# Optimization experiments

Hardware: AMD Instinct MI355X
Metric: run time of the kernel (lower is better)

Reference implementation:

```python
import jax, jax.numpy as jnp
import numpy as np

THRESHOLD = 0.3
STRENGTH = 0.1
MIN_S = 0.0
MAX_S = 0.5
EPS_COS = 1e-8
EPS_LN = 1e-5

B, T, D = 1024, 64, 256
P = 2048
H = 512


def _layernorm(x, g, b):
    mu = x.mean(-1, keepdims=True)
    var = ((x - mu) ** 2).mean(-1, keepdims=True)
    return (x - mu) * jax.lax.rsqrt(var + EPS_LN) * g + b


def setup_inputs() -> dict:
    key = jax.random.key(0)
    ks = jax.random.split(key, 10)
    s = lambda fan_in: 1.0 / np.sqrt(fan_in)
    return {
        "current_feat": jax.random.normal(ks[0], (B, T, D), jnp.float32),
        "prototype": jax.random.normal(ks[1], (P, T, D), jnp.float32),
        "dd_w1": jax.random.normal(ks[2], (2 * D, H), jnp.float32) * s(2 * D),
        "dd_b1": jnp.zeros((H,), jnp.float32),
        "dd_g1": jnp.ones((H,), jnp.float32),
        "dd_be1": jnp.zeros((H,), jnp.float32),
        "dd_w2": jax.random.normal(ks[3], (H, H // 2), jnp.float32) * s(H),
        "dd_b2": jnp.zeros((H // 2,), jnp.float32),
        "dd_w3": jax.random.normal(ks[4], (H // 2, 1), jnp.float32) * s(H // 2),
        "dd_b3": jnp.zeros((1,), jnp.float32),
        "cal_w1": jax.random.normal(ks[5], (D, H), jnp.float32) * s(D),
        "cal_b1": jnp.zeros((H,), jnp.float32),
        "cal_g1": jnp.ones((H,), jnp.float32),
        "cal_be1": jnp.zeros((H,), jnp.float32),
        "cal_w2": jax.random.normal(ks[6], (H, H), jnp.float32) * s(H),
        "cal_b2": jnp.zeros((H,), jnp.float32),
        "cal_w3": jax.random.normal(ks[7], (H, D), jnp.float32) * s(H),
        "cal_b3": jnp.zeros((D,), jnp.float32),
    }


def reference(current_feat, prototype,
              dd_w1, dd_b1, dd_g1, dd_be1, dd_w2, dd_b2, dd_w3, dd_b3,
              cal_w1, cal_b1, cal_g1, cal_be1, cal_w2, cal_b2, cal_w3, cal_b3):
    # --- drift detection ---
    feat_flat = current_feat.mean(axis=1)          # [B, D]
    proto_centers = prototype.mean(axis=1)         # [P, D]
    fn = jnp.maximum(jnp.linalg.norm(feat_flat, axis=-1), EPS_COS)   # [B]
    pn = jnp.maximum(jnp.linalg.norm(proto_centers, axis=-1), EPS_COS)  # [P]
    sim = jnp.einsum('bd,pd->bp', feat_flat, proto_centers) / (fn[:, None] * pn[None, :])
    drift_score = 1.0 - sim                        # [B, P]
    is_drifted = drift_score.mean(axis=0) > THRESHOLD  # [P] bool

    # --- calibration (batched over all P, then masked scatter) ---
    global_mean = feat_flat.mean(axis=0)           # [D]
    concat = jnp.concatenate(
        [proto_centers, jnp.broadcast_to(global_mean, (proto_centers.shape[0], global_mean.shape[0]))], axis=-1)  # [P, 2D]
    h = jax.nn.relu(_layernorm(concat @ dd_w1 + dd_b1, dd_g1, dd_be1))
    h = jax.nn.relu(h @ dd_w2 + dd_b2)
    drift_conf = jax.nn.sigmoid(h @ dd_w3 + dd_b3)[:, 0]  # [P]

    c = jax.nn.relu(_layernorm(proto_centers @ cal_w1 + cal_b1, cal_g1, cal_be1))
    c = jax.nn.relu(c @ cal_w2 + cal_b2)
    delta = c @ cal_w3 + cal_b3                    # [P, D]

    strength = jnp.clip(STRENGTH * drift_conf, MIN_S, MAX_S)  # [P]
    new_center = proto_centers + strength[:, None] * delta    # [P, D]

    calibrated = jnp.where(is_drifted[:, None, None], new_center[:, None, :], prototype)  # [P, T, D]
    return calibrated, drift_score, is_drifted
```

## Files before the change

### kernel.cpp

```cpp
#include <hip/hip_runtime.h>
#include <hip/hip_bf16.h>
#include <math.h>

#define BB 1024
#define TT 64
#define DD 256
#define PP 2048
#define HH 512

typedef __attribute__((ext_vector_type(8))) short short8;
typedef __attribute__((ext_vector_type(4))) short short4v;
typedef __attribute__((ext_vector_type(4))) float f32x4;

__device__ __forceinline__ float4 f4add(float4 a, float4 b) {
    return make_float4(a.x + b.x, a.y + b.y, a.z + b.z, a.w + b.w);
}

__device__ __forceinline__ void nt_store4(float* p, float4 v) {
    f32x4 t = {v.x, v.y, v.z, v.w};
    __builtin_nontemporal_store(t, (f32x4*)p);
}

__device__ __forceinline__ void nt_store1(float* p, float v) {
    __builtin_nontemporal_store(v, p);
}

__device__ __forceinline__ float4 nt_load4(const float* p) {
    f32x4 t = __builtin_nontemporal_load((const f32x4*)p);
    return make_float4(t.x, t.y, t.z, t.w);
}

__device__ __forceinline__ void store_bf16x4(__hip_bfloat16* dst, float4 m) {
    union { __hip_bfloat16 h[4]; short4v s; } u;
    u.h[0] = __float2bfloat16(m.x); u.h[1] = __float2bfloat16(m.y);
    u.h[2] = __float2bfloat16(m.z); u.h[3] = __float2bfloat16(m.w);
    *(short4v*)dst = u.s;
}

__global__ void prep_k(const float* __restrict__ cf, const float* __restrict__ proto,
                       const float* __restrict__ dd_w1, const float* __restrict__ dd_w2,
                       const float* __restrict__ cal_w1, const float* __restrict__ cal_w2,
                       const float* __restrict__ cal_w3,
                       float* __restrict__ ffm, float* __restrict__ fn,
                       float* __restrict__ pn, float* __restrict__ pc,
                       float* __restrict__ colsum,
                       __hip_bfloat16* __restrict__ ffb, __hip_bfloat16* __restrict__ pcb,
                       __hip_bfloat16* __restrict__ w1cat, __hip_bfloat16* __restrict__ w2dd,
                       __hip_bfloat16* __restrict__ w2cal, __hip_bfloat16* __restrict__ w3cal) {
    int b = blockIdx.x, tid = threadIdx.x;
    if (b < 768) {
        int wv = tid >> 6, lane = tid & 63;
        int row = (b << 2) + wv;
        const float* base = (row < 1024) ? cf + (size_t)row * TT * DD
                                         : proto + (size_t)(row - 1024) * TT * DD;
        const float* p = base + (lane << 2);
        float4 acc = make_float4(0.f, 0.f, 0.f, 0.f);
        float4 v[16];
        #pragma unroll
        for (int tb = 0; tb < TT; tb += 16) {
            #pragma unroll
            for (int i = 0; i < 16; ++i)
                v[i] = nt_load4(p + (size_t)(tb + i) * DD);
            #pragma unroll
            for (int i = 0; i < 8; ++i) v[i] = f4add(v[i], v[i + 8]);
            #pragma unroll
            for (int i = 0; i < 4; ++i) v[i] = f4add(v[i], v[i + 4]);
            acc = f4add(acc, f4add(f4add(v[0], v[1]), f4add(v[2], v[3])));
        }
        float4 m = make_float4(acc.x * (1.f / TT), acc.y * (1.f / TT),
                               acc.z * (1.f / TT), acc.w * (1.f / TT));
        if (row < 1024) {
            *(float4*)(ffm + (size_t)row * DD + (lane << 2)) = m;
            store_bf16x4(ffb + (size_t)row * DD + (lane << 2), m);
        } else {
            int r = row - 1024;
            *(float4*)(pc + (size_t)r * DD + (lane << 2)) = m;
            store_bf16x4(pcb + (size_t)r * DD + (lane << 2), m);
        }
        float q = m.x * m.x + m.y * m.y + m.z * m.z + m.w * m.w;
        #pragma unroll
        for (int o = 32; o > 0; o >>= 1) q += __shfl_xor(q, o, 64);
        if (lane == 0) {
            float nv = fmaxf(sqrtf(q), 1e-8f);
            if (row < 1024) fn[row] = nv; else pn[row - 1024] = nv;
        }
    } else {
        int bb = b - 768;
        if (bb < 8) colsum[bb * 256 + tid] = 0.f;
        #pragma unroll
        for (int i2 = 0; i2 < 4; ++i2) {
            int idx = bb * 1024 + i2 * 256 + tid;
            if (idx < 262144) {
                int half = idx >> 17;
                int i = idx & 131071;
                int n = i & 511, k = i >> 9;
                const float* src = half ? cal_w1 : dd_w1;
                float x = __builtin_nontemporal_load(src + (size_t)k * 512 + n);
                w1cat[(size_t)(half * 512 + n) * 256 + k] = __float2bfloat16(x);
            } else if (idx < 393216) {
                int i = idx - 262144;
                int n = i & 255, k = i >> 8;
                float x = __builtin_nontemporal_load(dd_w2 + (size_t)k * 256 + n);
                w2dd[(size_t)n * 512 + k] = __float2bfloat16(x);
            } else if (idx < 655360) {
                int i = idx - 393216;
                int n = i & 511, k = i >> 9;
                float x = __builtin_nontemporal_load(cal_w2 + (size_t)k * 512 + n);
                w2cal[(size_t)n * 512 + k] = __float2bfloat16(x);
            } else {
                int i = idx - 655360;
                int n = i & 255, k = i >> 8;
                float x = __builtin_nontemporal_load(cal_w3 + (size_t)k * 256 + n);
                w3cal[(size_t)n * 512 + k] = __float2bfloat16(x);
            }
        }
    }
}

__global__ void sim_addvec_k(const __hip_bfloat16* __restrict__ A,
                             const __hip_bfloat16* __restrict__ Bt,
                             const float* __restrict__ fn, const float* __restrict__ pn,
                             const float* __restrict__ ffm,
                             const float* __restrict__ dd_w1, const float* __restrict__ dd_b1,
                             float* __restrict__ drift, float* __restrict__ colsum,
                             float* __restrict__ addvec) {
    if (blockIdx.x >= 512) {
        __shared__ float gmk[256];
        int tid = threadIdx.x;
        const float* f = ffm + tid;
        float a0 = 0.f, a1 = 0.f, a2 = 0.f, a3 = 0.f, a4 = 0.f, a5 = 0.f, a6 = 0.f, a7 = 0.f;
        #pragma unroll 4
        for (int b = 0; b < 1024; b += 8) {
            a0 += f[(b + 0) << 8]; a1 += f[(b + 1) << 8];
            a2 += f[(b + 2) << 8]; a3 += f[(b + 3) << 8];
            a4 += f[(b + 4) << 8]; a5 += f[(b + 5) << 8];
            a6 += f[(b + 6) << 8]; a7 += f[(b + 7) << 8];
        }
        gmk[tid] = (((a0 + a1) + (a2 + a3)) + ((a4 + a5) + (a6 + a7))) * (1.f / BB);
        __syncthreads();
        int j = (blockIdx.x - 512) * 256 + tid;
        float s = dd_b1[j];
        #pragma unroll 8
        for (int k = 0; k < 256; ++k) s = fmaf(gmk[k], dd_w1[(size_t)(256 + k) * 512 + j], s);
        addvec[j] = s;
        return;
    }
    int wid = (blockIdx.x << 2) + (threadIdx.x >> 6);
    int lane = threadIdx.x & 63;
    int mw = wid >> 6, nw = wid & 63;
    int m0 = mw << 5, n0 = nw << 5;
    int lr = lane & 15, quad = lane >> 4;
    const __hip_bfloat16* pa0 = A + (size_t)(m0 + lr) * DD + quad * 8;
    const __hip_bfloat16* pa1 = pa0 + 16 * DD;
    const __hip_bfloat16* pb0 = Bt + (size_t)(n0 + lr) * DD + quad * 8;
    const __hip_bfloat16* pb1 = pb0 + 16 * DD;
    f32x4 acc00 = {0,0,0,0}, acc01 = {0,0,0,0}, acc10 = {0,0,0,0}, acc11 = {0,0,0,0};
    #pragma unroll
    for (int k = 0; k < DD; k += 32) {
        short8 a0 = *(const short8*)(pa0 + k);
        short8 a1 = *(const short8*)(pa1 + k);
        short8 b0 = *(const short8*)(pb0 + k);
        short8 b1 = *(const short8*)(pb1 + k);
        acc00 = __builtin_amdgcn_mfma_f32_16x16x32_bf16(a0, b0, acc00, 0, 0, 0);
        acc01 = __builtin_amdgcn_mfma_f32_16x16x32_bf16(a0, b1, acc01, 0, 0, 0);
        acc10 = __builtin_amdgcn_mfma_f32_16x16x32_bf16(a1, b0, acc10, 0, 0, 0);
        acc11 = __builtin_amdgcn_mfma_f32_16x16x32_bf16(a1, b1, acc11, 0, 0, 0);
    }
    int col0 = n0 + lr, col1 = col0 + 16;
    float ip0 = 1.f / pn[col0], ip1 = 1.f / pn[col1];
    float cs0 = 0.f, cs1 = 0.f;
    #pragma unroll
    for (int r = 0; r < 4; ++r) {
        int row0 = m0 + quad * 4 + r;
        int row1 = row0 + 16;
        float if0 = 1.f / fn[row0];
        float if1 = 1.f / fn[row1];
        float d00 = 1.f - acc00[r] * if0 * ip0;
        float d01 = 1.f - acc01[r] * if0 * ip1;
        float d10 = 1.f - acc10[r] * if1 * ip0;
        float d11 = 1.f - acc11[r] * if1 * ip1;
        nt_store1(&drift[(size_t)row0 * PP + col0], d00);
        nt_store1(&drift[(size_t)row0 * PP + col1], d01);
        nt_store1(&drift[(size_t)row1 * PP + col0], d10);
        nt_store1(&drift[(size_t)row1 * PP + col1], d11);
        cs0 += d00 + d10;
        cs1 += d01 + d11;
    }
    cs0 += __shfl_xor(cs0, 16, 64); cs0 += __shfl_xor(cs0, 32, 64);
    cs1 += __shfl_xor(cs1, 16, 64); cs1 += __shfl_xor(cs1, 32, 64);
    if (quad == 0) {
        atomicAdd(&colsum[col0], cs0);
        atomicAdd(&colsum[col1], cs1);
    }
}

#define LS 520
__global__ void __launch_bounds__(256)
mlp_k(const __hip_bfloat16* __restrict__ pcb,
      const __hip_bfloat16* __restrict__ w1cat,
      const float* __restrict__ addvec, const float* __restrict__ cal_b1,
      const float* __restrict__ gdd, const float* __restrict__ bedd,
      const float* __restrict__ gcal, const float* __restrict__ becal,
      const __hip_bfloat16* __restrict__ w2dd, const __hip_bfloat16* __restrict__ w2cal,
      const float* __restrict__ dd_b2, const float* __restrict__ cal_b2,
      const __hip_bfloat16* __restrict__ w3cal, const float* __restrict__ cal_b3,
      const float* __restrict__ dd_w3, const float* __restrict__ dd_b3,
      float* __restrict__ delta, float* __restrict__ strength) {
    __shared__ __hip_bfloat16 act1[32 * LS];
    __shared__ __hip_bfloat16 act2[32 * LS];
    __shared__ float lds_s[4][32];
    __shared__ float lds_q[4][32];

    int h  = blockIdx.x & 1;
    int r0 = (blockIdx.x >> 1) << 5;
    int wv = threadIdx.x >> 6;
    int lane = threadIdx.x & 63;
    int lr = lane & 15, quad = lane >> 4;

    const float* bias1 = h ? cal_b1 : addvec;
    const float* g  = h ? gcal : gdd;
    const float* be = h ? becal : bedd;

    const __hip_bfloat16* pa0 = pcb + (size_t)(r0 + lr) * DD + quad * 8;
    const __hip_bfloat16* pa1 = pa0 + 16 * DD;
    f32x4 a00[4], a01[4], a10[4], a11[4];
    float bi0[4], bi1[4];
    #pragma unroll
    for (int t = 0; t < 4; ++t) {
        int n0g = h * 512 + wv * 128 + t * 32;
        const __hip_bfloat16* pb0 = w1cat + (size_t)(n0g + lr) * DD + quad * 8;
        const __hip_bfloat16* pb1 = pb0 + 16 * DD;
        f32x4 c00 = {0,0,0,0}, c01 = {0,0,0,0}, c10 = {0,0,0,0}, c11 = {0,0,0,0};
        #pragma unroll
        for (int k = 0; k < DD; k += 32) {
            short8 av0 = *(const short8*)(pa0 + k);
            short8 av1 = *(const short8*)(pa1 + k);
            short8 bv0 = *(const short8*)(pb0 + k);
            short8 bv1 = *(const short8*)(pb1 + k);
            c00 = __builtin_amdgcn_mfma_f32_16x16x32_bf16(av0, bv0, c00, 0, 0, 0);
            c01 = __builtin_amdgcn_mfma_f32_16x16x32_bf16(av0, bv1, c01, 0, 0, 0);
            c10 = __builtin_amdgcn_mfma_f32_16x16x32_bf16(av1, bv0, c10, 0, 0, 0);
            c11 = __builtin_amdgcn_mfma_f32_16x16x32_bf16(av1, bv1, c11, 0, 0, 0);
        }
        a00[t] = c00; a01[t] = c01; a10[t] = c10; a11[t] = c11;
        int cl0 = wv * 128 + t * 32 + lr;
        bi0[t] = bias1[cl0];
        bi1[t] = bias1[cl0 + 16];
    }
    float ps_lo[4] = {0,0,0,0}, pq_lo[4] = {0,0,0,0};
    float ps_hi[4] = {0,0,0,0}, pq_hi[4] = {0,0,0,0};
    #pragma unroll
    for (int t = 0; t < 4; ++t) {
        #pragma unroll
        for (int r = 0; r < 4; ++r) {
            float v00 = a00[t][r] + bi0[t];
            float v01 = a01[t][r] + bi1[t];
            float v10 = a10[t][r] + bi0[t];
            float v11 = a11[t][r] + bi1[t];
            a00[t][r] = v00; a01[t][r] = v01; a10[t][r] = v10; a11[t][r] = v11;
            ps_lo[r] += v00 + v01;  pq_lo[r] += v00 * v00 + v01 * v01;
            ps_hi[r] += v10 + v11;  pq_hi[r] += v10 * v10 + v11 * v11;
        }
    }
    #pragma unroll
    for (int mset = 1; mset < 16; mset <<= 1) {
        #pragma unroll
        for (int r = 0; r < 4; ++r) {
            ps_lo[r] += __shfl_xor(ps_lo[r], mset, 64);
            pq_lo[r] += __shfl_xor(pq_lo[r], mset, 64);
            ps_hi[r] += __shfl_xor(ps_hi[r], mset, 64);
            pq_hi[r] += __shfl_xor(pq_hi[r], mset, 64);
        }
    }
    if (lr < 8) {
        int rr = quad * 4 + (lr & 3) + ((lr >> 2) << 4);
        lds_s[wv][rr] = (lr >= 4) ? ps_hi[lr & 3] : ps_lo[lr & 3];
        lds_q[wv][rr] = (lr >= 4) ? pq_hi[lr & 3] : pq_lo[lr & 3];
    }
    __syncthreads();

    float mu_lo[4], rs_lo[4], mu_hi[4], rs_hi[4];
    #pragma unroll
    for (int r = 0; r < 4; ++r) {
        int rl = quad * 4 + r;
        float s = lds_s[0][rl] + lds_s[1][rl] + lds_s[2][rl] + lds_s[3][rl];
        float q = lds_q[0][rl] + lds_q[1][rl] + lds_q[2][rl] + lds_q[3][rl];
        float mu = s * (1.f / HH);
        float var = fmaxf(q * (1.f / HH) - mu * mu, 0.f);
        mu_lo[r] = mu; rs_lo[r] = rsqrtf(var + 1e-5f);
        int rh = rl + 16;
        s = lds_s[0][rh] + lds_s[1][rh] + lds_s[2][rh] + lds_s[3][rh];
        q = lds_q[0][rh] + lds_q[1][rh] + lds_q[2][rh] + lds_q[3][rh];
        mu = s * (1.f / HH);
        var = fmaxf(q * (1.f / HH) - mu * mu, 0.f);
        mu_hi[r] = mu; rs_hi[r] = rsqrtf(var + 1e-5f);
    }
    #pragma unroll
    for (int t = 0; t < 4; ++t) {
        int c0 = wv * 128 + t * 32 + lr, c1 = c0 + 16;
        float g0 = g[c0], g1 = g[c1], b0 = be[c0], b1 = be[c1];
        #pragma unroll
        for (int r = 0; r < 4; ++r) {
            int rl = quad * 4 + r, rh = rl + 16;
            act1[rl * LS + c0] = __float2bfloat16(fmaxf((a00[t][r] - mu_lo[r]) * rs_lo[r] * g0 + b0, 0.f));
            act1[rl * LS + c1] = __float2bfloat16(fmaxf((a01[t][r] - mu_lo[r]) * rs_lo[r] * g1 + b1, 0.f));
            act1[rh * LS + c0] = __float2bfloat16(fmaxf((a10[t][r] - mu_hi[r]) * rs_hi[r] * g0 + b0, 0.f));
            act1[rh * LS + c1] = __float2bfloat16(fmaxf((a11[t][r] - mu_hi[r]) * rs_hi[r] * g1 + b1, 0.f));
        }
    }
    __syncthreads();

    {
        const __hip_bfloat16* w2 = h ? w2cal : w2dd;
        const float* b2 = h ? cal_b2 : dd_b2;
        int nt2 = h ? 4 : 2;
        #pragma unroll
        for (int tt = 0; tt < 4; ++tt) {
            if (tt < nt2) {
                int n0 = wv * (nt2 << 5) + (tt << 5);
                const __hip_bfloat16* pb0 = w2 + (size_t)(n0 + lr) * 512 + quad * 8;
                const __hip_bfloat16* pb1 = pb0 + 16 * 512;
                f32x4 c00 = {0,0,0,0}, c01 = {0,0,0,0}, c10 = {0,0,0,0}, c11 = {0,0,0,0};
                #pragma unroll
                for (int k = 0; k < 512; k += 32) {
                    short8 av0 = *(const short8*)&act1[lr * LS + quad * 8 + k];
                    short8 av1 = *(const short8*)&act1[(lr + 16) * LS + quad * 8 + k];
                    short8 bv0 = *(const short8*)(pb0 + k);
                    short8 bv1 = *(const short8*)(pb1 + k);
                    c00 = __builtin_amdgcn_mfma_f32_16x16x32_bf16(av0, bv0, c00, 0, 0, 0);
                    c01 = __builtin_amdgcn_mfma_f32_16x16x32_bf16(av0, bv1, c01, 0, 0, 0);
                    c10 = __builtin_amdgcn_mfma_f32_16x16x32_bf16(av1, bv0, c10, 0, 0, 0);
                    c11 = __builtin_amdgcn_mfma_f32_16x16x32_bf16(av1, bv1, c11, 0, 0, 0);
                }
                float bb0 = b2[n0 + lr], bb1 = b2[n0 + 16 + lr];
                #pragma unroll
                for (int r = 0; r < 4; ++r) {
                    int rl = quad * 4 + r, rh = rl + 16;
                    act2[rl * LS + n0 + lr]      = __float2bfloat16(fmaxf(c00[r] + bb0, 0.f));
                    act2[rl * LS + n0 + 16 + lr] = __float2bfloat16(fmaxf(c01[r] + bb1, 0.f));
                    act2[rh * LS + n0 + lr]      = __float2bfloat16(fmaxf(c10[r] + bb0, 0.f));
                    act2[rh * LS + n0 + 16 + lr] = __float2bfloat16(fmaxf(c11[r] + bb1, 0.f));
                }
            }
        }
    }
    __syncthreads();

    if (h == 0) {
        int r = threadIdx.x >> 3, e = threadIdx.x & 7;
        float s = 0.f;
        #pragma unroll 8
        for (int c = 0; c < 32; ++c) {
            int cc = e * 32 + c;
            s += __bfloat162float(act2[r * LS + cc]) * dd_w3[cc];
        }
        s += __shfl_down(s, 4, 8);
        s += __shfl_down(s, 2, 8);
        s += __shfl_down(s, 1, 8);
        if (e == 0) {
            float conf = 1.f / (1.f + expf(-(s + dd_b3[0])));
            strength[r0 + r] = fminf(fmaxf(0.1f * conf, 0.f), 0.5f);
        }
    } else {
        #pragma unroll
        for (int tt = 0; tt < 2; ++tt) {
            int n0 = (wv << 6) + (tt << 5);
            const __hip_bfloat16* pb0 = w3cal + (size_t)(n0 + lr) * 512 + quad * 8;
            const __hip_bfloat16* pb1 = pb0 + 16 * 512;
            f32x4 c00 = {0,0,0,0}, c01 = {0,0,0,0}, c10 = {0,0,0,0}, c11 = {0,0,0,0};
            #pragma unroll
            for (int k = 0; k < 512; k += 32) {
                short8 av0 = *(const short8*)&act2[lr * LS + quad * 8 + k];
                short8 av1 = *(const short8*)&act2[(lr + 16) * LS + quad * 8 + k];
                short8 bv0 = *(const short8*)(pb0 + k);
                short8 bv1 = *(const short8*)(pb1 + k);
                c00 = __builtin_amdgcn_mfma_f32_16x16x32_bf16(av0, bv0, c00, 0, 0, 0);
                c01 = __builtin_amdgcn_mfma_f32_16x16x32_bf16(av0, bv1, c01, 0, 0, 0);
                c10 = __builtin_amdgcn_mfma_f32_16x16x32_bf16(av1, bv0, c10, 0, 0, 0);
                c11 = __builtin_amdgcn_mfma_f32_16x16x32_bf16(av1, bv1, c11, 0, 0, 0);
            }
            float bb0 = cal_b3[n0 + lr], bb1 = cal_b3[n0 + 16 + lr];
            #pragma unroll
            for (int r = 0; r < 4; ++r) {
                int rl = quad * 4 + r, rh = rl + 16;
                delta[(size_t)(r0 + rl) * 256 + n0 + lr]      = c00[r] + bb0;
                delta[(size_t)(r0 + rl) * 256 + n0 + 16 + lr] = c01[r] + bb1;
                delta[(size_t)(r0 + rh) * 256 + n0 + lr]      = c10[r] + bb0;
                delta[(size_t)(r0 + rh) * 256 + n0 + 16 + lr] = c11[r] + bb1;
            }
        }
    }
}

__global__ void finalize_k(const float* __restrict__ pc, const float* __restrict__ delta,
                           const float* __restrict__ strength, const float* __restrict__ colsum,
                           const float* __restrict__ proto, float* __restrict__ out,
                           float* __restrict__ out_is) {
    int p = blockIdx.x;
    int d4 = (threadIdx.x & 63) << 2;
    int t0 = threadIdx.x >> 6;
    bool dr = colsum[p] * (1.f / BB) > 0.3f;
    if (threadIdx.x == 0) out_is[p] = dr ? 1.f : 0.f;
    float* o = out + (size_t)p * TT * DD;
    if (dr) {
        float s = strength[p];
        float4 pcv = *(const float4*)(pc + (size_t)p * DD + d4);
        float4 dv  = *(const float4*)(delta + (size_t)p * DD + d4);
        float4 nc = make_float4(fmaf(s, dv.x, pcv.x), fmaf(s, dv.y, pcv.y),
                                fmaf(s, dv.z, pcv.z), fmaf(s, dv.w, pcv.w));
        #pragma unroll
        for (int t = t0; t < TT; t += 4)
            nt_store4(o + t * DD + d4, nc);
    } else {
        const float* pr = proto + (size_t)p * TT * DD;
        #pragma unroll
        for (int t = t0; t < TT; t += 4)
            nt_store4(o + t * DD + d4, nt_load4(pr + t * DD + d4));
    }
}

extern "C" void kernel_launch(void* const* d_in, const int* in_sizes, int n_in,
                              void* d_out, int out_size, void* d_ws, size_t ws_size,
                              hipStream_t stream) {
    const float* cf     = (const float*)d_in[0];
    const float* proto  = (const float*)d_in[1];
    const float* dd_w1  = (const float*)d_in[2];
    const float* dd_b1  = (const float*)d_in[3];
    const float* dd_g1  = (const float*)d_in[4];
    const float* dd_be1 = (const float*)d_in[5];
    const float* dd_w2  = (const float*)d_in[6];
    const float* dd_b2  = (const float*)d_in[7];
    const float* dd_w3  = (const float*)d_in[8];
    const float* dd_b3  = (const float*)d_in[9];
    const float* cal_w1 = (const float*)d_in[10];
    const float* cal_b1 = (const float*)d_in[11];
    const float* cal_g1 = (const float*)d_in[12];
    const float* cal_be1= (const float*)d_in[13];
    const float* cal_w2 = (const float*)d_in[14];
    const float* cal_b2 = (const float*)d_in[15];
    const float* cal_w3 = (const float*)d_in[16];
    const float* cal_b3 = (const float*)d_in[17];

    float* out_cal   = (float*)d_out;
    float* out_drift = out_cal + (size_t)PP * TT * DD;
    float* out_is    = out_drift + (size_t)BB * PP;

    float* w = (float*)d_ws;
    float* colsum   = w;
    float* addvec   = w + 4096;
    float* fn       = w + 4608;
    float* pn       = w + 5632;
    float* strength = w + 7680;
    float* pc       = w + 9728;
    float* ffm      = w + 534016;
    float* delta    = w + 2631168;
    __hip_bfloat16* bb = (__hip_bfloat16*)(w + 3155456);
    __hip_bfloat16* ffb     = bb;
    __hip_bfloat16* pcb     = bb + 262144;
    __hip_bfloat16* w1cat   = bb + 786432;
    __hip_bfloat16* w2dd    = bb + 1048576;
    __hip_bfloat16* w2cal   = bb + 1179648;
    __hip_bfloat16* w3cal   = bb + 1441792;

    prep_k<<<1536, 256, 0, stream>>>(cf, proto, dd_w1, dd_w2, cal_w1, cal_w2, cal_w3,
                                     ffm, fn, pn, pc, colsum, ffb, pcb,
                                     w1cat, w2dd, w2cal, w3cal);
    sim_addvec_k<<<514, 256, 0, stream>>>(ffb, pcb, fn, pn, ffm, dd_w1, dd_b1,
                                          out_drift, colsum, addvec);
    mlp_k<<<128, 256, 0, stream>>>(pcb, w1cat, addvec, cal_b1,
                                   dd_g1, dd_be1, cal_g1, cal_be1,
                                   w2dd, w2cal, dd_b2, cal_b2,
                                   w3cal, cal_b3, dd_w3, dd_b3,
                                   delta, strength);
    finalize_k<<<PP, 256, 0, stream>>>(pc, delta, strength, colsum, proto, out_cal, out_is);
}
```

Measured before the change: 399.7 us.

## Fuse similarity GEMM into MLP kernel and stage mean-reduction through LDS

Changes the prep kernel so each block reduces one full [T,D] row, staging it into LDS with global_load_lds direct-to-LDS copies, instead of having one wave per row. The similarity GEMM and the MLP become a single launch: blocks 0-127 run the MLP and compute the global mean and addvec locally in h==0 blocks, while the remaining blocks run the similarity tiles. This removes one kernel launch and one dependency boundary, and lets the MLP overlap with the drift GEMM. In exchange, each MLP block recomputes the global mean over all 1024 rows, and the prep kernel now uses 66KB+ of LDS per block, which lowers occupancy on the bandwidth-bound mean pass.

```diff
diff --git a/kernel.cpp b/kernel.cpp
--- a/kernel.cpp
+++ b/kernel.cpp
@@ -11,10 +11,8 @@
 typedef __attribute__((ext_vector_type(8))) short short8;
 typedef __attribute__((ext_vector_type(4))) short short4v;
 typedef __attribute__((ext_vector_type(4))) float f32x4;
-
-__device__ __forceinline__ float4 f4add(float4 a, float4 b) {
-    return make_float4(a.x + b.x, a.y + b.y, a.z + b.z, a.w + b.w);
-}
+typedef __attribute__((address_space(3))) void as3_void;
+typedef const __attribute__((address_space(1))) void as1_cvoid;
 
 __device__ __forceinline__ void nt_store4(float* p, float4 v) {
     f32x4 t = {v.x, v.y, v.z, v.w};
@@ -30,62 +28,62 @@
     return make_float4(t.x, t.y, t.z, t.w);
 }
 
-__device__ __forceinline__ void store_bf16x4(__hip_bfloat16* dst, float4 m) {
-    union { __hip_bfloat16 h[4]; short4v s; } u;
-    u.h[0] = __float2bfloat16(m.x); u.h[1] = __float2bfloat16(m.y);
-    u.h[2] = __float2bfloat16(m.z); u.h[3] = __float2bfloat16(m.w);
-    *(short4v*)dst = u.s;
-}
-
-__global__ void prep_k(const float* __restrict__ cf, const float* __restrict__ proto,
-                       const float* __restrict__ dd_w1, const float* __restrict__ dd_w2,
-                       const float* __restrict__ cal_w1, const float* __restrict__ cal_w2,
-                       const float* __restrict__ cal_w3,
-                       float* __restrict__ ffm, float* __restrict__ fn,
-                       float* __restrict__ pn, float* __restrict__ pc,
-                       float* __restrict__ colsum,
-                       __hip_bfloat16* __restrict__ ffb, __hip_bfloat16* __restrict__ pcb,
-                       __hip_bfloat16* __restrict__ w1cat, __hip_bfloat16* __restrict__ w2dd,
-                       __hip_bfloat16* __restrict__ w2cal, __hip_bfloat16* __restrict__ w3cal) {
+__global__ void __launch_bounds__(256)
+prep_k(const float* __restrict__ cf, const float* __restrict__ proto,
+       const float* __restrict__ dd_w1, const float* __restrict__ dd_w2,
+       const float* __restrict__ cal_w1, const float* __restrict__ cal_w2,
+       const float* __restrict__ cal_w3,
+       float* __restrict__ ffm, float* __restrict__ fn,
+       float* __restrict__ pn, float* __restrict__ pc,
+       float* __restrict__ colsum,
+       __hip_bfloat16* __restrict__ ffb, __hip_bfloat16* __restrict__ pcb,
+       __hip_bfloat16* __restrict__ w1cat, __hip_bfloat16* __restrict__ w2dd,
+       __hip_bfloat16* __restrict__ w2cal, __hip_bfloat16* __restrict__ w3cal) {
+    __shared__ float tile[TT * DD];
+    __shared__ float smr[1024];
     int b = blockIdx.x, tid = threadIdx.x;
-    if (b < 768) {
+    if (b < 3072) {
         int wv = tid >> 6, lane = tid & 63;
-        int row = (b << 2) + wv;
-        const float* base = (row < 1024) ? cf + (size_t)row * TT * DD
-                                         : proto + (size_t)(row - 1024) * TT * DD;
-        const float* p = base + (lane << 2);
-        float4 acc = make_float4(0.f, 0.f, 0.f, 0.f);
-        float4 v[16];
-        #pragma unroll
-        for (int tb = 0; tb < TT; tb += 16) {
-            #pragma unroll
-            for (int i = 0; i < 16; ++i)
-                v[i] = nt_load4(p + (size_t)(tb + i) * DD);
-            #pragma unroll
-            for (int i = 0; i < 8; ++i) v[i] = f4add(v[i], v[i + 8]);
-            #pragma unroll
-            for (int i = 0; i < 4; ++i) v[i] = f4add(v[i], v[i + 4]);
-            acc = f4add(acc, f4add(f4add(v[0], v[1]), f4add(v[2], v[3])));
-        }
-        float4 m = make_float4(acc.x * (1.f / TT), acc.y * (1.f / TT),
-                               acc.z * (1.f / TT), acc.w * (1.f / TT));
-        if (row < 1024) {
-            *(float4*)(ffm + (size_t)row * DD + (lane << 2)) = m;
-            store_bf16x4(ffb + (size_t)row * DD + (lane << 2), m);
+        const float* base = (b < 1024) ? cf + (size_t)b * TT * DD
+                                       : proto + (size_t)(b - 1024) * TT * DD;
+        #pragma unroll
+        for (int j = 0; j < 16; ++j) {
+            int t = (wv << 4) + j;
+            __builtin_amdgcn_global_load_lds(
+                (as1_cvoid*)(base + (t << 8) + (lane << 2)),
+                (as3_void*)&tile[t << 8], 16, 0, 0);
+        }
+        __syncthreads();
+        int c4 = tid & 63, t0 = tid >> 6;
+        float4 s = make_float4(0.f, 0.f, 0.f, 0.f);
+        #pragma unroll
+        for (int t = t0; t < TT; t += 4) {
+            float4 v = *(const float4*)&tile[(t << 8) + (c4 << 2)];
+            s.x += v.x; s.y += v.y; s.z += v.z; s.w += v.w;
+        }
+        *(float4*)&smr[(t0 << 8) + (c4 << 2)] = s;
+        __syncthreads();
+        float m = (smr[tid] + smr[256 + tid] + smr[512 + tid] + smr[768 + tid]) * (1.f / TT);
+        if (b < 1024) {
+            ffm[(size_t)b * DD + tid] = m;
+            ffb[(size_t)b * DD + tid] = __float2bfloat16(m);
         } else {
-            int r = row - 1024;
-            *(float4*)(pc + (size_t)r * DD + (lane << 2)) = m;
-            store_bf16x4(pcb + (size_t)r * DD + (lane << 2), m);
-        }
-        float q = m.x * m.x + m.y * m.y + m.z * m.z + m.w * m.w;
+            int r = b - 1024;
+            pc[(size_t)r * DD + tid] = m;
+            pcb[(size_t)r * DD + tid] = __float2bfloat16(m);
+        }
+        __syncthreads();
+        float q = m * m;
         #pragma unroll
         for (int o = 32; o > 0; o >>= 1) q += __shfl_xor(q, o, 64);
-        if (lane == 0) {
-            float nv = fmaxf(sqrtf(q), 1e-8f);
-            if (row < 1024) fn[row] = nv; else pn[row - 1024] = nv;
+        if (lane == 0) smr[wv] = q;
+        __syncthreads();
+        if (tid == 0) {
+            float nv = fmaxf(sqrtf(smr[0] + smr[1] + smr[2] + smr[3]), 1e-8f);
+            if (b < 1024) fn[b] = nv; else pn[b - 1024] = nv;
         }
     } else {
-        int bb = b - 768;
+        int bb = b - 3072;
         if (bb < 8) colsum[bb * 256 + tid] = 0.f;
         #pragma unroll
         for (int i2 = 0; i2 < 4; ++i2) {
@@ -117,111 +115,116 @@
     }
 }
 
-__global__ void sim_addvec_k(const __hip_bfloat16* __restrict__ A,
-                             const __hip_bfloat16* __restrict__ Bt,
-                             const float* __restrict__ fn, const float* __restrict__ pn,
-                             const float* __restrict__ ffm,
-                             const float* __restrict__ dd_w1, const float* __restrict__ dd_b1,
-                             float* __restrict__ drift, float* __restrict__ colsum,
-                             float* __restrict__ addvec) {
-    if (blockIdx.x >= 512) {
-        __shared__ float gmk[256];
-        int tid = threadIdx.x;
-        const float* f = ffm + tid;
-        float a0 = 0.f, a1 = 0.f, a2 = 0.f, a3 = 0.f, a4 = 0.f, a5 = 0.f, a6 = 0.f, a7 = 0.f;
-        #pragma unroll 4
-        for (int b = 0; b < 1024; b += 8) {
-            a0 += f[(b + 0) << 8]; a1 += f[(b + 1) << 8];
-            a2 += f[(b + 2) << 8]; a3 += f[(b + 3) << 8];
-            a4 += f[(b + 4) << 8]; a5 += f[(b + 5) << 8];
-            a6 += f[(b + 6) << 8]; a7 += f[(b + 7) << 8];
-        }
-        gmk[tid] = (((a0 + a1) + (a2 + a3)) + ((a4 + a5) + (a6 + a7))) * (1.f / BB);
-        __syncthreads();
-        int j = (blockIdx.x - 512) * 256 + tid;
-        float s = dd_b1[j];
-        #pragma unroll 8
-        for (int k = 0; k < 256; ++k) s = fmaf(gmk[k], dd_w1[(size_t)(256 + k) * 512 + j], s);
-        addvec[j] = s;
-        return;
-    }
-    int wid = (blockIdx.x << 2) + (threadIdx.x >> 6);
-    int lane = threadIdx.x & 63;
-    int mw = wid >> 6, nw = wid & 63;
-    int m0 = mw << 5, n0 = nw << 5;
-    int lr = lane & 15, quad = lane >> 4;
-    const __hip_bfloat16* pa0 = A + (size_t)(m0 + lr) * DD + quad * 8;
-    const __hip_bfloat16* pa1 = pa0 + 16 * DD;
-    const __hip_bfloat16* pb0 = Bt + (size_t)(n0 + lr) * DD + quad * 8;
-    const __hip_bfloat16* pb1 = pb0 + 16 * DD;
-    f32x4 acc00 = {0,0,0,0}, acc01 = {0,0,0,0}, acc10 = {0,0,0,0}, acc11 = {0,0,0,0};
-    #pragma unroll
-    for (int k = 0; k < DD; k += 32) {
-        short8 a0 = *(const short8*)(pa0 + k);
-        short8 a1 = *(const short8*)(pa1 + k);
-        short8 b0 = *(const short8*)(pb0 + k);
-        short8 b1 = *(const short8*)(pb1 + k);
-        acc00 = __builtin_amdgcn_mfma_f32_16x16x32_bf16(a0, b0, acc00, 0, 0, 0);
-        acc01 = __builtin_amdgcn_mfma_f32_16x16x32_bf16(a0, b1, acc01, 0, 0, 0);
-        acc10 = __builtin_amdgcn_mfma_f32_16x16x32_bf16(a1, b0, acc10, 0, 0, 0);
-        acc11 = __builtin_amdgcn_mfma_f32_16x16x32_bf16(a1, b1, acc11, 0, 0, 0);
-    }
-    int col0 = n0 + lr, col1 = col0 + 16;
-    float ip0 = 1.f / pn[col0], ip1 = 1.f / pn[col1];
-    float cs0 = 0.f, cs1 = 0.f;
-    #pragma unroll
-    for (int r = 0; r < 4; ++r) {
-        int row0 = m0 + quad * 4 + r;
-        int row1 = row0 + 16;
-        float if0 = 1.f / fn[row0];
-        float if1 = 1.f / fn[row1];
-        float d00 = 1.f - acc00[r] * if0 * ip0;
-        float d01 = 1.f - acc01[r] * if0 * ip1;
-        float d10 = 1.f - acc10[r] * if1 * ip0;
-        float d11 = 1.f - acc11[r] * if1 * ip1;
-        nt_store1(&drift[(size_t)row0 * PP + col0], d00);
-        nt_store1(&drift[(size_t)row0 * PP + col1], d01);
-        nt_store1(&drift[(size_t)row1 * PP + col0], d10);
-        nt_store1(&drift[(size_t)row1 * PP + col1], d11);
-        cs0 += d00 + d10;
-        cs1 += d01 + d11;
-    }
-    cs0 += __shfl_xor(cs0, 16, 64); cs0 += __shfl_xor(cs0, 32, 64);
-    cs1 += __shfl_xor(cs1, 16, 64); cs1 += __shfl_xor(cs1, 32, 64);
-    if (quad == 0) {
-        atomicAdd(&colsum[col0], cs0);
-        atomicAdd(&colsum[col1], cs1);
-    }
-}
-
 #define LS 520
 __global__ void __launch_bounds__(256)
-mlp_k(const __hip_bfloat16* __restrict__ pcb,
-      const __hip_bfloat16* __restrict__ w1cat,
-      const float* __restrict__ addvec, const float* __restrict__ cal_b1,
-      const float* __restrict__ gdd, const float* __restrict__ bedd,
-      const float* __restrict__ gcal, const float* __restrict__ becal,
-      const __hip_bfloat16* __restrict__ w2dd, const __hip_bfloat16* __restrict__ w2cal,
-      const float* __restrict__ dd_b2, const float* __restrict__ cal_b2,
-      const __hip_bfloat16* __restrict__ w3cal, const float* __restrict__ cal_b3,
-      const float* __restrict__ dd_w3, const float* __restrict__ dd_b3,
-      float* __restrict__ delta, float* __restrict__ strength) {
+simmlp_k(const __hip_bfloat16* __restrict__ A,
+         const __hip_bfloat16* __restrict__ Bt,
+         const float* __restrict__ fn, const float* __restrict__ pn,
+         const float* __restrict__ ffm,
+         const float* __restrict__ dd_w1, const float* __restrict__ dd_b1,
+         const __hip_bfloat16* __restrict__ w1cat, const float* __restrict__ cal_b1,
+         const float* __restrict__ gdd, const float* __restrict__ bedd,
+         const float* __restrict__ gcal, const float* __restrict__ becal,
+         const __hip_bfloat16* __restrict__ w2dd, const __hip_bfloat16* __restrict__ w2cal,
+         const float* __restrict__ dd_b2, const float* __restrict__ cal_b2,
+         const __hip_bfloat16* __restrict__ w3cal, const float* __restrict__ cal_b3,
+         const float* __restrict__ dd_w3, const float* __restrict__ dd_b3,
+         float* __restrict__ drift, float* __restrict__ colsum,
+         float* __restrict__ delta, float* __restrict__ strength) {
     __shared__ __hip_bfloat16 act1[32 * LS];
     __shared__ __hip_bfloat16 act2[32 * LS];
+    __shared__ float scratch[1024];
+    __shared__ float gmk[256];
+    __shared__ float addv[512];
     __shared__ float lds_s[4][32];
     __shared__ float lds_q[4][32];
 
+    int tid = threadIdx.x;
+    int wv = tid >> 6;
+    int lane = tid & 63;
+    int lr = lane & 15, quad = lane >> 4;
+
+    if (blockIdx.x >= 128) {
+        int wid = ((blockIdx.x - 128) << 2) + wv;
+        int mw = wid >> 6, nw = wid & 63;
+        int m0 = mw << 5, n0 = nw << 5;
+        const __hip_bfloat16* pa0 = A + (size_t)(m0 + lr) * DD + quad * 8;
+        const __hip_bfloat16* pa1 = pa0 + 16 * DD;
+        const __hip_bfloat16* pb0 = Bt + (size_t)(n0 + lr) * DD + quad * 8;
+        const __hip_bfloat16* pb1 = pb0 + 16 * DD;
+        f32x4 acc00 = {0,0,0,0}, acc01 = {0,0,0,0}, acc10 = {0,0,0,0}, acc11 = {0,0,0,0};
+        #pragma unroll
+        for (int k = 0; k < DD; k += 32) {
+            short8 a0 = *(const short8*)(pa0 + k);
+            short8 a1 = *(const short8*)(pa1 + k);
+            short8 b0 = *(const short8*)(pb0 + k);
+            short8 b1 = *(const short8*)(pb1 + k);
+            acc00 = __builtin_amdgcn_mfma_f32_16x16x32_bf16(a0, b0, acc00, 0, 0, 0);
+            acc01 = __builtin_amdgcn_mfma_f32_16x16x32_bf16(a0, b1, acc01, 0, 0, 0);
+            acc10 = __builtin_amdgcn_mfma_f32_16x16x32_bf16(a1, b0, acc10, 0, 0, 0);
+            acc11 = __builtin_amdgcn_mfma_f32_16x16x32_bf16(a1, b1, acc11, 0, 0, 0);
+        }
+        int col0 = n0 + lr, col1 = col0 + 16;
+        float ip0 = 1.f / pn[col0], ip1 = 1.f / pn[col1];
+        float cs0 = 0.f, cs1 = 0.f;
+        #pragma unroll
+        for (int r = 0; r < 4; ++r) {
+            int row0 = m0 + quad * 4 + r;
+            int row1 = row0 + 16;
+            float if0 = 1.f / fn[row0];
+            float if1 = 1.f / fn[row1];
+            float d00 = 1.f - acc00[r] * if0 * ip0;
+            float d01 = 1.f - acc01[r] * if0 * ip1;
+            float d10 = 1.f - acc10[r] * if1 * ip0;
+            float d11 = 1.f - acc11[r] * if1 * ip1;
+            nt_store1(&drift[(size_t)row0 * PP + col0], d00);
+            nt_store1(&drift[(size_t)row0 * PP + col1], d01);
+            nt_store1(&drift[(size_t)row1 * PP + col0], d10);
+            nt_store1(&drift[(size_t)row1 * PP + col1], d11);
+            cs0 += d00 + d10;
+            cs1 += d01 + d11;
+        }
+        cs0 += __shfl_xor(cs0, 16, 64); cs0 += __shfl_xor(cs0, 32, 64);
+        cs1 += __shfl_xor(cs1, 16, 64); cs1 += __shfl_xor(cs1, 32, 64);
+        if (quad == 0) {
+            atomicAdd(&colsum[col0], cs0);
+            atomicAdd(&colsum[col1], cs1);
+        }
+        return;
+    }
+
     int h  = blockIdx.x & 1;
     int r0 = (blockIdx.x >> 1) << 5;
-    int wv = threadIdx.x >> 6;
-    int lane = threadIdx.x & 63;
-    int lr = lane & 15, quad = lane >> 4;
-
-    const float* bias1 = h ? cal_b1 : addvec;
     const float* g  = h ? gcal : gdd;
     const float* be = h ? becal : bedd;
 
-    const __hip_bfloat16* pa0 = pcb + (size_t)(r0 + lr) * DD + quad * 8;
+    if (h == 0) {
+        int c4 = tid & 63, rg = tid >> 6;
+        float4 a = make_float4(0.f, 0.f, 0.f, 0.f);
+        const float* f = ffm + (size_t)(rg << 8) * DD + (c4 << 2);
+        #pragma unroll 8
+        for (int i = 0; i < 256; ++i) {
+            float4 v = *(const float4*)(f + (size_t)i * DD);
+            a.x += v.x; a.y += v.y; a.z += v.z; a.w += v.w;
+        }
+        *(float4*)&scratch[(rg << 8) + (c4 << 2)] = a;
+        __syncthreads();
+        gmk[tid] = (scratch[tid] + scratch[256 + tid] + scratch[512 + tid] + scratch[768 + tid])
+                   * (1.f / BB);
+        __syncthreads();
+        float s0 = dd_b1[tid], s1 = dd_b1[tid + 256];
+        #pragma unroll 8
+        for (int k = 0; k < 256; ++k) {
+            float gm = gmk[k];
+            s0 = fmaf(gm, dd_w1[(size_t)(256 + k) * 512 + tid], s0);
+            s1 = fmaf(gm, dd_w1[(size_t)(256 + k) * 512 + tid + 256], s1);
+        }
+        addv[tid] = s0;
+        addv[tid + 256] = s1;
+        __syncthreads();
+    }
+
+    const __hip_bfloat16* pa0 = Bt + (size_t)(r0 + lr) * DD + quad * 8;
     const __hip_bfloat16* pa1 = pa0 + 16 * DD;
     f32x4 a00[4], a01[4], a10[4], a11[4];
     float bi0[4], bi1[4];
@@ -244,8 +247,8 @@
         }
         a00[t] = c00; a01[t] = c01; a10[t] = c10; a11[t] = c11;
         int cl0 = wv * 128 + t * 32 + lr;
-        bi0[t] = bias1[cl0];
-        bi1[t] = bias1[cl0 + 16];
+        bi0[t] = h ? cal_b1[cl0] : addv[cl0];
+        bi1[t] = h ? cal_b1[cl0 + 16] : addv[cl0 + 16];
     }
     float ps_lo[4] = {0,0,0,0}, pq_lo[4] = {0,0,0,0};
     float ps_hi[4] = {0,0,0,0}, pq_hi[4] = {0,0,0,0};
@@ -347,7 +350,7 @@
     __syncthreads();
 
     if (h == 0) {
-        int r = threadIdx.x >> 3, e = threadIdx.x & 7;
+        int r = tid >> 3, e = tid & 7;
         float s = 0.f;
         #pragma unroll 8
         for (int c = 0; c < 32; ++c) {
@@ -447,7 +450,6 @@
 
     float* w = (float*)d_ws;
     float* colsum   = w;
-    float* addvec   = w + 4096;
     float* fn       = w + 4608;
     float* pn       = w + 5632;
     float* strength = w + 7680;
@@ -462,15 +464,14 @@
     __hip_bfloat16* w2cal   = bb + 1179648;
     __hip_bfloat16* w3cal   = bb + 1441792;
 
-    prep_k<<<1536, 256, 0, stream>>>(cf, proto, dd_w1, dd_w2, cal_w1, cal_w2, cal_w3,
+    prep_k<<<3840, 256, 0, stream>>>(cf, proto, dd_w1, dd_w2, cal_w1, cal_w2, cal_w3,
                                      ffm, fn, pn, pc, colsum, ffb, pcb,
                                      w1cat, w2dd, w2cal, w3cal);
-    sim_addvec_k<<<514, 256, 0, stream>>>(ffb, pcb, fn, pn, ffm, dd_w1, dd_b1,
-                                          out_drift, colsum, addvec);
-    mlp_k<<<128, 256, 0, stream>>>(pcb, w1cat, addvec, cal_b1,
-                                   dd_g1, dd_be1, cal_g1, cal_be1,
-                                   w2dd, w2cal, dd_b2, cal_b2,
-                                   w3cal, cal_b3, dd_w3, dd_b3,
-                                   delta, strength);
+    simmlp_k<<<640, 256, 0, stream>>>(ffb, pcb, fn, pn, ffm, dd_w1, dd_b1,
+                                      w1cat, cal_b1,
+                                      dd_g1, dd_be1, cal_g1, cal_be1,
+                                      w2dd, w2cal, dd_b2, cal_b2,
+                                      w3cal, cal_b3, dd_w3, dd_b3,
+                                      out_drift, colsum, delta, strength);
     finalize_k<<<PP, 256, 0, stream>>>(pc, delta, strength, colsum, proto, out_cal, out_is);
 }
```

Result: faster. 378.4 us (-5.3%).
